# Kernel tuning notes

Measured on AMD Instinct MI355X. Metric: run time of the kernel, lower is better.

## Reference

```python
import jax, jax.numpy as jnp
import numpy as np

FD_EPS = 1e-4
MAX_ITERATIONS = 30


def _fd_path_gradient(p, eps):
    """Vectorized central finite-difference gradient of the local path-length cost.

    Faithful to the torch loop: for each interior t and each dim d,
    cost(t) = ||p[t]-p[t-1]|| + ||p[t+1]-p[t]|| with p[t,d] perturbed by +/-eps.
    """
    B, T, D = p.shape
    a = p[:, 1:-1, :] - p[:, :-2, :]   # [B, T-2, D] back segment
    b = p[:, 2:, :] - p[:, 1:-1, :]    # [B, T-2, D] forward segment
    pert = eps * jnp.eye(D, dtype=p.dtype)  # [D, D] one perturbation per dim
    # perturbing p[t,d] by +eps adds eps*e_d to a and subtracts it from b
    cp = jnp.linalg.norm(a[:, :, None, :] + pert, axis=-1) \
       + jnp.linalg.norm(b[:, :, None, :] - pert, axis=-1)  # [B, T-2, D]
    cm = jnp.linalg.norm(a[:, :, None, :] - pert, axis=-1) \
       + jnp.linalg.norm(b[:, :, None, :] + pert, axis=-1)
    g = (cp - cm) / (2.0 * eps)
    # boundary points (t=0, t=T-1) get zero gradient, as in the torch code
    return jnp.pad(g, ((0, 0), (1, 1), (0, 0)))


def setup_inputs() -> dict:
    key = jax.random.key(0)
    k1, k2, k3 = jax.random.split(key, 3)
    B, T, D = 32, 256, 32
    return {
        "path": jax.random.normal(k1, (B, T, D), dtype=jnp.float32),
        "metric_field": jax.random.normal(k2, (B, T, D, D), dtype=jnp.float32),
        "affordance": jax.random.normal(k3, (B, T), dtype=jnp.float32),
        "step_size": jnp.float32(0.01),   # nn.Parameter
        "momentum": jnp.float32(0.9),     # nn.Parameter
    }


def reference(path, metric_field, affordance, step_size, momentum):
    # metric_field and affordance are accepted but unused by the cost,
    # exactly as in the original module.
    del metric_field, affordance

    def step(carry, _):
        p, v = carry
        g = _fd_path_gradient(p, FD_EPS)
        v = momentum * v - step_size * g
        p = p + v
        # pin endpoints to the original path
        p = p.at[:, 0].set(path[:, 0]).at[:, -1].set(path[:, -1])
        return (p, v), None

    init = (path, jnp.zeros_like(path))
    (p_opt, _), _ = jax.lax.scan(step, init, None, length=MAX_ITERATIONS)
    return p_opt
```

## Files before the change

kernel.cpp:

```cpp
#include <hip/hip_runtime.h>

#define GEO_T  256
#define GEO_D  32
#define ITERS  30
#define CHUNKS 16
#define OWNW   16
#define HALO   8
#define WIN    32

__device__ __forceinline__ float qsum(float x) {
    x += __int_as_float(__builtin_amdgcn_mov_dpp(__float_as_int(x), 0xB1, 0xF, 0xF, true));
    x += __int_as_float(__builtin_amdgcn_mov_dpp(__float_as_int(x), 0x4E, 0xF, 0xF, true));
    return x;
}

__global__ __launch_bounds__(64)
void geodesic_kernel(const float* __restrict__ path,
                     const float* __restrict__ step_p,
                     const float* __restrict__ mom_p,
                     float* __restrict__ out)
{
    const int blk   = blockIdx.x;
    const int b     = blk >> 4;
    const int chunk = blk & 15;
    const int lane  = threadIdx.x;
    const int Q     = lane >> 2;
    const int d8    = (lane & 3) * 8;

    const int own_lo = 1 + OWNW * chunk;
    const int own_hi = min(own_lo + OWNW, GEO_T - 1);
    int ws = own_lo - HALO;
    if (ws < 0) ws = 0;
    if (ws > GEO_T - WIN) ws = GEO_T - WIN;

    const int r0 = ws + 2 * Q;
    const int r1 = r0 + 1;

    const bool upd0 = (Q != 0);
    const bool upd1 = (Q != 15);

    const float eta = step_p[0];
    const float mom = mom_p[0];

    const float* pb = path + (size_t)b * GEO_T * GEO_D;
    float p0[8], p1[8], v0[8], v1[8];
    {
        float4 x0 = *(const float4*)&pb[r0 * GEO_D + d8];
        float4 x1 = *(const float4*)&pb[r0 * GEO_D + d8 + 4];
        float4 y0 = *(const float4*)&pb[r1 * GEO_D + d8];
        float4 y1 = *(const float4*)&pb[r1 * GEO_D + d8 + 4];
        p0[0]=x0.x; p0[1]=x0.y; p0[2]=x0.z; p0[3]=x0.w;
        p0[4]=x1.x; p0[5]=x1.y; p0[6]=x1.z; p0[7]=x1.w;
        p1[0]=y0.x; p1[1]=y0.y; p1[2]=y0.z; p1[3]=y0.w;
        p1[4]=y1.x; p1[5]=y1.y; p1[6]=y1.z; p1[7]=y1.w;
    }
    #pragma unroll
    for (int d = 0; d < 8; ++d) { v0[d] = 0.f; v1[d] = 0.f; }

    const int lm4 = (lane - 4) & 63;
    const int lp4 = (lane + 4) & 63;

    #pragma unroll 2
    for (int it = 0; it < ITERS; ++it) {
        float pm[8], a0[8], a1[8];
        #pragma unroll
        for (int d = 0; d < 8; ++d) pm[d] = __shfl(p1[d], lm4, 64);

        float sa0 = 0.f, sa1 = 0.f;
        #pragma unroll
        for (int d = 0; d < 8; ++d) {
            a0[d] = p0[d] - pm[d];
            a1[d] = p1[d] - p0[d];
            sa0 = fmaf(a0[d], a0[d], sa0);
            sa1 = fmaf(a1[d], a1[d], sa1);
        }
        sa0 = qsum(sa0);
        sa1 = qsum(sa1);

        float bb[8];
        #pragma unroll
        for (int d = 0; d < 8; ++d) bb[d] = __shfl(a0[d], lp4, 64);
        float sb1 = __shfl(sa0, lp4, 64);

        const float ra0 = __builtin_amdgcn_rsqf(fmaxf(sa0, 1e-30f));
        const float ra1 = __builtin_amdgcn_rsqf(fmaxf(sa1, 1e-30f));
        const float rb1 = __builtin_amdgcn_rsqf(fmaxf(sb1, 1e-30f));
        const float e0 = eta * ra0, e1 = eta * ra1, eb = eta * rb1;

        if (upd0) {
            #pragma unroll
            for (int d = 0; d < 8; ++d) {
                v0[d] = fmaf(mom, v0[d], fmaf(e1, a1[d], -e0 * a0[d]));
                p0[d] += v0[d];
            }
        }
        if (upd1) {
            #pragma unroll
            for (int d = 0; d < 8; ++d) {
                v1[d] = fmaf(mom, v1[d], fmaf(eb, bb[d], -e1 * a1[d]));
                p1[d] += v1[d];
            }
        }
    }

    const bool w0 = (r0 >= own_lo && r0 < own_hi) || (chunk == 0 && r0 == 0);
    const bool w1 = (r1 >= own_lo && r1 < own_hi) || (chunk == CHUNKS - 1 && r1 == GEO_T - 1);
    float* ob = out + (size_t)b * GEO_T * GEO_D;
    if (w0) {
        *(float4*)&ob[r0 * GEO_D + d8]     = make_float4(p0[0], p0[1], p0[2], p0[3]);
        *(float4*)&ob[r0 * GEO_D + d8 + 4] = make_float4(p0[4], p0[5], p0[6], p0[7]);
    }
    if (w1) {
        *(float4*)&ob[r1 * GEO_D + d8]     = make_float4(p1[0], p1[1], p1[2], p1[3]);
        *(float4*)&ob[r1 * GEO_D + d8 + 4] = make_float4(p1[4], p1[5], p1[6], p1[7]);
    }
}

extern "C" void kernel_launch(void* const* d_in, const int* in_sizes, int n_in,
                              void* d_out, int out_size, void* d_ws, size_t ws_size,
                              hipStream_t stream) {
    const float* path   = (const float*)d_in[0];
    const float* step_p = (const float*)d_in[3];
    const float* mom_p  = (const float*)d_in[4];
    float* out = (float*)d_out;

    const int B = in_sizes[0] / (GEO_T * GEO_D);
    geodesic_kernel<<<B * CHUNKS, 64, 0, stream>>>(path, step_p, mom_p, out);
}
```

Baseline: 15.34 us.

## Transpose lane mapping so neighbor exchange uses DPP row shifts, packed float2 math

Lanes now map row-pair index to the low 4 bits and the dimension group to the high bits. Neighboring time rows are therefore adjacent lanes within a DPP row, so the ds_bpermute shuffles become row_shr/row_shl DPP moves. Each lane computes the forward segment locally, and the cross-dimension norm reduction switches to ds_swizzle xor16 plus permlane32_swap. Arithmetic is repacked into float2 vectors so it can use packed FP32 instructions. This trades LDS-path shuffles for cheaper cross-lane ops, but it relies on the gfx950 permlane32_swap builtin and on DPP bound_ctrl giving zero at row edges, which only matters for the lanes whose updates are masked.

Result: faster. 14.97 us (-2.4%).

```diff
diff --git a/kernel.cpp b/kernel.cpp
--- a/kernel.cpp
+++ b/kernel.cpp
@@ -8,10 +8,22 @@
 #define HALO   8
 #define WIN    32
 
-__device__ __forceinline__ float qsum(float x) {
-    x += __int_as_float(__builtin_amdgcn_mov_dpp(__float_as_int(x), 0xB1, 0xF, 0xF, true));
-    x += __int_as_float(__builtin_amdgcn_mov_dpp(__float_as_int(x), 0x4E, 0xF, 0xF, true));
-    return x;
+typedef float v2f __attribute__((ext_vector_type(2)));
+
+__device__ __forceinline__ v2f splat2(float s) { v2f r; r[0] = s; r[1] = s; return r; }
+
+__device__ __forceinline__ float dpp_shr1(float x) {
+    return __int_as_float(__builtin_amdgcn_mov_dpp(__float_as_int(x), 0x111, 0xF, 0xF, true));
+}
+__device__ __forceinline__ float dpp_shl1(float x) {
+    return __int_as_float(__builtin_amdgcn_mov_dpp(__float_as_int(x), 0x101, 0xF, 0xF, true));
+}
+__device__ __forceinline__ float xor16_add(float x) {
+    return x + __int_as_float(__builtin_amdgcn_ds_swizzle(__float_as_int(x), 0x401F));
+}
+__device__ __forceinline__ float xor32_add(float x) {
+    auto r = __builtin_amdgcn_permlane32_swap(__float_as_int(x), __float_as_int(x), false, false);
+    return __int_as_float(r[0]) + __int_as_float(r[1]);
 }
 
 __global__ __launch_bounds__(64)
@@ -24,8 +36,9 @@
     const int b     = blk >> 4;
     const int chunk = blk & 15;
     const int lane  = threadIdx.x;
-    const int Q     = lane >> 2;
-    const int d8    = (lane & 3) * 8;
+    const int i     = lane & 15;
+    const int dg    = lane >> 4;
+    const int d8    = dg * 8;
 
     const int own_lo = 1 + OWNW * chunk;
     const int own_hi = min(own_lo + OWNW, GEO_T - 1);
@@ -33,72 +46,74 @@
     if (ws < 0) ws = 0;
     if (ws > GEO_T - WIN) ws = GEO_T - WIN;
 
-    const int r0 = ws + 2 * Q;
+    const int r0 = ws + 2 * i;
     const int r1 = r0 + 1;
-
-    const bool upd0 = (Q != 0);
-    const bool upd1 = (Q != 15);
+    const bool upd0 = (i != 0);
+    const bool upd1 = (i != 15);
 
     const float eta = step_p[0];
     const float mom = mom_p[0];
 
     const float* pb = path + (size_t)b * GEO_T * GEO_D;
-    float p0[8], p1[8], v0[8], v1[8];
+    v2f p0[4], p1[4], v0[4], v1[4];
     {
         float4 x0 = *(const float4*)&pb[r0 * GEO_D + d8];
         float4 x1 = *(const float4*)&pb[r0 * GEO_D + d8 + 4];
         float4 y0 = *(const float4*)&pb[r1 * GEO_D + d8];
         float4 y1 = *(const float4*)&pb[r1 * GEO_D + d8 + 4];
-        p0[0]=x0.x; p0[1]=x0.y; p0[2]=x0.z; p0[3]=x0.w;
-        p0[4]=x1.x; p0[5]=x1.y; p0[6]=x1.z; p0[7]=x1.w;
-        p1[0]=y0.x; p1[1]=y0.y; p1[2]=y0.z; p1[3]=y0.w;
-        p1[4]=y1.x; p1[5]=y1.y; p1[6]=y1.z; p1[7]=y1.w;
+        p0[0][0]=x0.x; p0[0][1]=x0.y; p0[1][0]=x0.z; p0[1][1]=x0.w;
+        p0[2][0]=x1.x; p0[2][1]=x1.y; p0[3][0]=x1.z; p0[3][1]=x1.w;
+        p1[0][0]=y0.x; p1[0][1]=y0.y; p1[1][0]=y0.z; p1[1][1]=y0.w;
+        p1[2][0]=y1.x; p1[2][1]=y1.y; p1[3][0]=y1.z; p1[3][1]=y1.w;
     }
     #pragma unroll
-    for (int d = 0; d < 8; ++d) { v0[d] = 0.f; v1[d] = 0.f; }
-
-    const int lm4 = (lane - 4) & 63;
-    const int lp4 = (lane + 4) & 63;
+    for (int k = 0; k < 4; ++k) { v0[k] = splat2(0.f); v1[k] = splat2(0.f); }
 
     #pragma unroll 2
     for (int it = 0; it < ITERS; ++it) {
-        float pm[8], a0[8], a1[8];
+        v2f pm[4], pn[4];
         #pragma unroll
-        for (int d = 0; d < 8; ++d) pm[d] = __shfl(p1[d], lm4, 64);
+        for (int k = 0; k < 4; ++k) {
+            pm[k][0] = dpp_shr1(p1[k][0]);  pm[k][1] = dpp_shr1(p1[k][1]);
+            pn[k][0] = dpp_shl1(p0[k][0]);  pn[k][1] = dpp_shl1(p0[k][1]);
+        }
 
-        float sa0 = 0.f, sa1 = 0.f;
+        v2f a0[4], a1[4], bb[4];
+        v2f s0 = splat2(0.f), s1 = splat2(0.f);
         #pragma unroll
-        for (int d = 0; d < 8; ++d) {
-            a0[d] = p0[d] - pm[d];
-            a1[d] = p1[d] - p0[d];
-            sa0 = fmaf(a0[d], a0[d], sa0);
-            sa1 = fmaf(a1[d], a1[d], sa1);
+        for (int k = 0; k < 4; ++k) {
+            a0[k] = p0[k] - pm[k];
+            a1[k] = p1[k] - p0[k];
+            bb[k] = pn[k] - p1[k];
+            s0 = a0[k] * a0[k] + s0;
+            s1 = a1[k] * a1[k] + s1;
         }
-        sa0 = qsum(sa0);
-        sa1 = qsum(sa1);
-
-        float bb[8];
-        #pragma unroll
-        for (int d = 0; d < 8; ++d) bb[d] = __shfl(a0[d], lp4, 64);
-        float sb1 = __shfl(sa0, lp4, 64);
+        float sa0 = xor32_add(xor16_add(s0[0] + s0[1]));
+        float sa1 = xor32_add(xor16_add(s1[0] + s1[1]));
+        float sb1 = dpp_shl1(sa0);
 
         const float ra0 = __builtin_amdgcn_rsqf(fmaxf(sa0, 1e-30f));
         const float ra1 = __builtin_amdgcn_rsqf(fmaxf(sa1, 1e-30f));
         const float rb1 = __builtin_amdgcn_rsqf(fmaxf(sb1, 1e-30f));
-        const float e0 = eta * ra0, e1 = eta * ra1, eb = eta * rb1;
+        const v2f e0 = splat2(eta * ra0);
+        const v2f e1 = splat2(eta * ra1);
+        const v2f eb = splat2(eta * rb1);
+        const v2f mo = splat2(mom);
 
         if (upd0) {
             #pragma unroll
-            for (int d = 0; d < 8; ++d) {
-                v0[d] = fmaf(mom, v0[d], fmaf(e1, a1[d], -e0 * a0[d]));
-                p0[d] += v0[d];
+            for (int k = 0; k < 4; ++k) {
+                v2f g = a1[k] * e1 - a0[k] * e0;
+                v0[k] = v0[k] * mo + g;
+                p0[k] = p0[k] + v0[k];
             }
         }
         if (upd1) {
             #pragma unroll
-            for (int d = 0; d < 8; ++d) {
-                v1[d] = fmaf(mom, v1[d], fmaf(eb, bb[d], -e1 * a1[d]));
-                p1[d] += v1[d];
+            for (int k = 0; k < 4; ++k) {
+                v2f g = bb[k] * eb - a1[k] * e1;
+                v1[k] = v1[k] * mo + g;
+                p1[k] = p1[k] + v1[k];
             }
         }
     }
@@ -107,12 +122,12 @@
     const bool w1 = (r1 >= own_lo && r1 < own_hi) || (chunk == CHUNKS - 1 && r1 == GEO_T - 1);
     float* ob = out + (size_t)b * GEO_T * GEO_D;
     if (w0) {
-        *(float4*)&ob[r0 * GEO_D + d8]     = make_float4(p0[0], p0[1], p0[2], p0[3]);
-        *(float4*)&ob[r0 * GEO_D + d8 + 4] = make_float4(p0[4], p0[5], p0[6], p0[7]);
+        *(float4*)&ob[r0 * GEO_D + d8]     = make_float4(p0[0][0], p0[0][1], p0[1][0], p0[1][1]);
+        *(float4*)&ob[r0 * GEO_D + d8 + 4] = make_float4(p0[2][0], p0[2][1], p0[3][0], p0[3][1]);
     }
     if (w1) {
-        *(float4*)&ob[r1 * GEO_D + d8]     = make_float4(p1[0], p1[1], p1[2], p1[3]);
-        *(float4*)&ob[r1 * GEO_D + d8 + 4] = make_float4(p1[4], p1[5], p1[6], p1[7]);
+        *(float4*)&ob[r1 * GEO_D + d8]     = make_float4(p1[0][0], p1[0][1], p1[1][0], p1[1][1]);
+        *(float4*)&ob[r1 * GEO_D + d8 + 4] = make_float4(p1[2][0], p1[2][1], p1[3][0], p1[3][1]);
     }
 }
 
```
